# Performance work log

Hardware: AMD Instinct MI355X
Metric: run time of the kernel (lower is better)

The kernel has to match this reference:

```python
import jax, jax.numpy as jnp
import numpy as np

B, C, F = 4, 512, 2048
N, H = 8, 64  # header_size, header_channels
ALPHA = 1.0 / np.sqrt(H)


def setup_inputs() -> dict:
    key = jax.random.key(0)
    ks = jax.random.split(key, 6)
    return {
        "from_tensor": jax.random.normal(ks[0], (B, C, F), jnp.float32),
        "to_tensor": jax.random.normal(ks[1], (B, C, F), jnp.float32),
        "mask": jnp.ones((B, F, F), jnp.float32),
        "Wq": jax.random.normal(ks[2], (N * H, C), jnp.float32) * 0.02,
        "bq": jnp.zeros((N * H,), jnp.float32),
        "Wk": jax.random.normal(ks[3], (N * H, C), jnp.float32) * 0.02,
        "bk": jnp.zeros((N * H,), jnp.float32),
        "Wv": jax.random.normal(ks[4], (N * H, C), jnp.float32) * 0.02,
        "bv": jnp.zeros((N * H,), jnp.float32),
    }


def reference(from_tensor, to_tensor, mask, Wq, bq, Wk, bk, Wv, bv):
    b, _, f = from_tensor.shape
    t = to_tensor.shape[2]
    # Dense over channel dim: [B,C,F] -> [B,N*H,F], then split heads
    q = (jnp.einsum("oc,bcf->bof", Wq, from_tensor) + bq[None, :, None]).reshape(b, N, H, f)
    k = (jnp.einsum("oc,bct->bot", Wk, to_tensor) + bk[None, :, None]).reshape(b, N, H, t)
    v = (jnp.einsum("oc,bct->bot", Wv, to_tensor) + bv[None, :, None]).reshape(b, N, H, t)
    # score: q^T @ k -> [B,N,F,T]
    score = jnp.einsum("bnhf,bnht->bnft", q, k) * ALPHA
    score = score + (1.0 - mask[:, None]) * -100000.0
    probs = jax.nn.softmax(score, axis=-1)  # dropout=0 (inference)
    # context: probs @ v^T -> [B,N,F,H], transpose -> [B,N,H,F]
    ctx = jnp.einsum("bnft,bnht->bnhf", probs, v)
    return ctx.reshape(b, N * H, f)
```

## Files before the change

### kernel.cpp

```cpp
#include <hip/hip_runtime.h>

typedef __bf16 bf16x8 __attribute__((ext_vector_type(8)));
typedef float f32x4 __attribute__((ext_vector_type(4)));
typedef float f32x16 __attribute__((ext_vector_type(16)));
typedef unsigned short u16;
typedef u16 u16x8 __attribute__((ext_vector_type(8)));
typedef unsigned int u32;
typedef u32 u32x4 __attribute__((ext_vector_type(4)));
typedef unsigned long long u64;

#define DEVFN static __device__ __forceinline__

DEVFN u16 f2bf(float x) {
  u32 u = __builtin_bit_cast(u32, x);
  u32 r = u + 0x7FFFu + ((u >> 16) & 1u);
  return (u16)(r >> 16);
}

DEVFN float myexp2(float x) {
#if __has_builtin(__builtin_amdgcn_exp2f)
  return __builtin_amdgcn_exp2f(x);
#else
  return exp2f(x);
#endif
}

DEVFN u32 cvt_pk_bf16(float lo, float hi) {
  u32 r;
  asm("v_cvt_pk_bf16_f32 %0, %1, %2" : "=v"(r) : "v"(lo), "v"(hi));
  return r;
}

__global__ __launch_bounds__(256, 2) void proj_kernel(
    const float* __restrict__ from_t, const float* __restrict__ to_t,
    const float* __restrict__ Wq, const float* __restrict__ bq,
    const float* __restrict__ Wk, const float* __restrict__ bk,
    const float* __restrict__ Wv, const float* __restrict__ bv,
    u16* __restrict__ qt, u16* __restrict__ kt, u16* __restrict__ vt) {
  const int d     = blockIdx.x;
  const int xcd   = d & 7;
  const int b     = xcd >> 1;
  const int fh    = xcd & 1;
  const int local = d >> 3;
  const int mat   = local >> 5;
  const int o0    = ((local >> 3) & 3) * 128;
  const int f0    = (fh * 8 + (local & 7)) * 128;

  const float* X    = (mat == 0) ? from_t : to_t;
  const float* W    = (mat == 0) ? Wq : (mat == 1 ? Wk : Wv);
  const float* bias = (mat == 0) ? bq : (mat == 1 ? bk : bv);
  const bool isT = (mat < 2);

  __shared__ u16 Xs[128][64];
  __shared__ u16 Ws[128][64];

  const int tid  = threadIdx.x;
  const int lane = tid & 63;
  const int w    = tid >> 6;

  f32x4 acc[4][4];
#pragma unroll
  for (int i = 0; i < 4; ++i)
#pragma unroll
    for (int j = 0; j < 4; ++j)
#pragma unroll
      for (int r = 0; r < 4; ++r) acc[i][j][r] = 0.f;

  const int arow0 = (w & 1) * 64;
  const int brow0 = (w >> 1) * 64;

  for (int c0 = 0; c0 < 512; c0 += 64) {
    __syncthreads();
#pragma unroll
    for (int i = 0; i < 4; ++i) {
      const int task = tid + 256 * i;
      const int f = task & 127, cg = task >> 7;
      const float* xp = X + ((size_t)b * 512 + c0 + cg * 8) * 2048 + f0 + f;
      float xv[8];
#pragma unroll
      for (int j = 0; j < 8; ++j) xv[j] = xp[(size_t)j * 2048];
      u32x4 pk;
#pragma unroll
      for (int j = 0; j < 4; ++j) pk[j] = cvt_pk_bf16(xv[2 * j], xv[2 * j + 1]);
      *(u32x4*)&Xs[f][(cg ^ (f & 7)) * 8] = pk;
    }
#pragma unroll
    for (int i = 0; i < 4; ++i) {
      const int task = tid + 256 * i;
      const int o = task & 127, cg = task >> 7;
      const float* wp = W + (size_t)(o0 + o) * 512 + c0 + cg * 8;
      const float4 w0 = *(const float4*)(wp);
      const float4 w1 = *(const float4*)(wp + 4);
      u32x4 pk;
      pk[0] = cvt_pk_bf16(w0.x, w0.y);
      pk[1] = cvt_pk_bf16(w0.z, w0.w);
      pk[2] = cvt_pk_bf16(w1.x, w1.y);
      pk[3] = cvt_pk_bf16(w1.z, w1.w);
      *(u32x4*)&Ws[o][(cg ^ (o & 7)) * 8] = pk;
    }
    __syncthreads();

#pragma unroll
    for (int kk = 0; kk < 2; ++kk) {
      const int cb8 = kk * 4;
      bf16x8 afr[4], bfr[4];
#pragma unroll
      for (int mi = 0; mi < 4; ++mi) {
        const int row = arow0 + mi * 16 + (lane & 15);
        const int ch  = (cb8 + (lane >> 4)) ^ (row & 7);
        afr[mi] = *(const bf16x8*)&(isT ? Xs : Ws)[row][ch * 8];
      }
#pragma unroll
      for (int ni = 0; ni < 4; ++ni) {
        const int row = brow0 + ni * 16 + (lane & 15);
        const int ch  = (cb8 + (lane >> 4)) ^ (row & 7);
        bfr[ni] = *(const bf16x8*)&(isT ? Ws : Xs)[row][ch * 8];
      }
#pragma unroll
      for (int mi = 0; mi < 4; ++mi)
#pragma unroll
        for (int ni = 0; ni < 4; ++ni)
          acc[mi][ni] = __builtin_amdgcn_mfma_f32_16x16x32_bf16(
              afr[mi], bfr[ni], acc[mi][ni], 0, 0, 0);
    }
  }

  const float qscale = 0.18033688011112042f;
#pragma unroll
  for (int mi = 0; mi < 4; ++mi)
#pragma unroll
    for (int ni = 0; ni < 4; ++ni)
#pragma unroll
      for (int r = 0; r < 4; ++r) {
        const int rA = arow0 + mi * 16 + (lane >> 4) * 4 + r;
        const int cB = brow0 + ni * 16 + (lane & 15);
        int f, o;
        if (isT) { f = f0 + rA; o = o0 + cB; }
        else     { o = o0 + rA; f = f0 + cB; }
        float val = acc[mi][ni][r] + bias[o];
        if (mat == 0) val *= qscale;
        const u16 hv = f2bf(val);
        if (isT) {
          u16* dst = (mat == 0) ? qt : kt;
          dst[(((size_t)b * 8 + (o >> 6)) * 2048 + f) * 64 + (o & 63)] = hv;
        } else {
          vt[((size_t)b * 512 + o) * 2048 + f] = hv;
        }
      }
}

__global__ __launch_bounds__(256, 4) void maskflag_kernel(
    const float* __restrict__ mask, u32* __restrict__ fmask) {
  const int d    = blockIdx.x;
  const int b    = d >> 9;
  const int ft   = (d >> 5) & 15;
  const int tile = d & 31;
  const int t    = threadIdx.x;

  const float* base =
      mask + ((size_t)b * 2048 + ft * 128) * 2048 + tile * 64;
  bool ok = true;
#pragma unroll
  for (int i = 0; i < 8; ++i) {
    const int row = (t >> 4) * 8 + i;
    const float4 v = *(const float4*)(base + (size_t)row * 2048 + (t & 15) * 4);
    ok = ok && (v.x == 1.0f) && (v.y == 1.0f) && (v.z == 1.0f) && (v.w == 1.0f);
  }
  const u64 bal = __ballot(ok);
  __shared__ u32 wok[4];
  if ((t & 63) == 0) wok[t >> 6] = (bal == ~0ull) ? 1u : 0u;
  __syncthreads();
  if (t == 0) {
    const u32 allok = wok[0] & wok[1] & wok[2] & wok[3];
    if (allok) atomicOr(&fmask[b * 16 + ft], 1u << tile);
  }
}

#define SB __builtin_amdgcn_sched_barrier(0)

#define STAGE(BB, T0)                                                          \
  do {                                                                         \
    __builtin_amdgcn_global_load_lds(                                          \
        (const __attribute__((address_space(1))) void*)(ksrc1 + (size_t)(T0) * 64), \
        (__attribute__((address_space(3))) void*)&Ks[BB][w * 16][0], 16, 0, 0);\
    __builtin_amdgcn_global_load_lds(                                          \
        (const __attribute__((address_space(1))) void*)(ksrc2 + (size_t)(T0) * 64), \
        (__attribute__((address_space(3))) void*)&Ks[BB][w * 16 + 8][0], 16, 0, 0); \
    __builtin_amdgcn_global_load_lds(                                          \
        (const __attribute__((address_space(1))) void*)(vsrc1 + (T0)),         \
        (__attribute__((address_space(3))) void*)&Vs[BB][w * 16][0], 16, 0, 0);\
    __builtin_amdgcn_global_load_lds(                                          \
        (const __attribute__((address_space(1))) void*)(vsrc2 + (T0)),         \
        (__attribute__((address_space(3))) void*)&Vs[BB][w * 16 + 8][0], 16, 0, 0); \
  } while (0)

#define LDK(BUF)                                                               \
  do {                                                                         \
    _Pragma("unroll")                                                          \
    for (int kf_ = 0; kf_ < 4; ++kf_)                                          \
      _Pragma("unroll")                                                        \
      for (int mi_ = 0; mi_ < 2; ++mi_) {                                      \
        const int row_ = mi_ * 32 + fl;                                        \
        kreg[mi_][kf_] =                                                       \
            *(const bf16x8*)&Ks[BUF][row_][((kf_ * 2 + g) ^ (row_ & 7)) * 8];  \
      }                                                                        \
  } while (0)

#define LDV(BUF)                                                               \
  do {                                                                         \
    _Pragma("unroll")                                                          \
    for (int tf_ = 0; tf_ < 4; ++tf_)                                          \
      _Pragma("unroll")                                                        \
      for (int mh_ = 0; mh_ < 2; ++mh_) {                                      \
        const int row_ = mh_ * 32 + fl;                                        \
        vreg[mh_][tf_] =                                                       \
            *(const bf16x8*)&Vs[BUF][row_][((tf_ * 2 + g) ^ (row_ & 7)) * 8];  \
      }                                                                        \
  } while (0)

#define QKMM(SN)                                                               \
  do {                                                                         \
    _Pragma("unroll")                                                          \
    for (int m_ = 0; m_ < 2; ++m_)                                             \
      _Pragma("unroll")                                                        \
      for (int r_ = 0; r_ < 16; ++r_) SN[m_][r_] = 0.f;                        \
    _Pragma("unroll")                                                          \
    for (int kf_ = 0; kf_ < 4; ++kf_)                                          \
      _Pragma("unroll")                                                        \
      for (int mi_ = 0; mi_ < 2; ++mi_)                                        \
        SN[mi_] = __builtin_amdgcn_mfma_f32_32x32x16_bf16(kreg[mi_][kf_],      \
                                                          qf[kf_], SN[mi_],    \
                                                          0, 0, 0);            \
  } while (0)

#define ROUND(RB, SC, SN, T0)                                                  \
  {                                                                            \
    asm volatile("s_waitcnt vmcnt(0)" ::: "memory");                           \
    SB;                                                                        \
    __builtin_amdgcn_s_barrier();                                              \
    SB;                                                                        \
    LDV(RB);                                                                   \
    LDK((RB + 1) & 3);                                                         \
    SB;                                                                        \
    STAGE((RB + 2) & 3, ((T0) + 128) & 2047);                                  \
    SB;                                                                        \
    QKMM(SN);           \
                  \
    if (!((fmask >> ((T0) >> 6)) & 1u)) {                                      \
      float4 mk[8];                                                            \
      _Pragma("unroll")                                                        \
      for (int i_ = 0; i_ < 8; ++i_)                                           \
        mk[i_] = *(const float4*)(mrow + (T0) + (i_ >> 2) * 32 +               \
                                  (i_ & 3) * 8 + g * 4);                       \
      _Pragma("unroll")                                                        \
      for (int mi = 0; mi < 2; ++mi)                                           \
        _Pragma("unroll")                                                      \
        for (int q = 0; q < 4; ++q) {                                          \
          const float4 mv = mk[mi * 4 + q];                                    \
          SC[mi][q * 4 + 0] = fmaf(mv.x - 1.f, 144269.50408889634f, SC[mi][q * 4 + 0]); \
          SC[mi][q * 4 + 1] = fmaf(mv.y - 1.f, 144269.50408889634f, SC[mi][q * 4 + 1]); \
          SC[mi][q * 4 + 2] = fmaf(mv.z - 1.f, 144269.50408889634f, SC[mi][q * 4 + 2]); \
          SC[mi][q * 4 + 3] = fmaf(mv.w - 1.f, 144269.50408889634f, SC[mi][q * 4 + 3]); \
        }                                                                      \
    }                                                                          \
    float ps0 = 0.f, ps1 = 0.f, ps2 = 0.f, ps3 = 0.f;                          \
    _Pragma("unroll")                                                          \
    for (int mi = 0; mi < 2; ++mi)                                             \
      _Pragma("unroll")                                                        \
      for (int r = 0; r < 16; r += 4) {                                        \
        SC[mi][r + 0] = myexp2(SC[mi][r + 0]); ps0 += SC[mi][r + 0];           \
        SC[mi][r + 1] = myexp2(SC[mi][r + 1]); ps1 += SC[mi][r + 1];           \
        SC[mi][r + 2] = myexp2(SC[mi][r + 2]); ps2 += SC[mi][r + 2];           \
        SC[mi][r + 3] = myexp2(SC[mi][r + 3]); ps3 += SC[mi][r + 3];           \
      }                                                                        \
    {                                                                          \
      float ps = (ps0 + ps1) + (ps2 + ps3);                                    \
      ps += __shfl_xor(ps, 32, 64);                                            \
      L += ps;                                                                 \
    }                                                                          \
        \
    u32 dwv[2][4][2];                                                          \
    _Pragma("unroll")                                                          \
    for (int mi = 0; mi < 2; ++mi)                                             \
      _Pragma("unroll")                                                        \
      for (int q = 0; q < 4; ++q) {                                            \
        dwv[mi][q][0] = cvt_pk_bf16(SC[mi][q * 4 + 0], SC[mi][q * 4 + 1]);     \
        dwv[mi][q][1] = cvt_pk_bf16(SC[mi][q * 4 + 2], SC[mi][q * 4 + 3]);     \
      }                                                                        \
    _Pragma("unroll")                                                          \
    for (int tf = 0; tf < 4; ++tf) {                                           \
      const int m_ = tf >> 1, bq2 = tf & 1;                                    \
      u32 A0 = dwv[m_][bq2 * 2][0], A1 = dwv[m_][bq2 * 2][1];                  \
      u32 C0 = dwv[m_][bq2 * 2 + 1][0], C1 = dwv[m_][bq2 * 2 + 1][1];          \
      asm("v_permlane32_swap_b32 %0, %1" : "+v"(A0), "+v"(C0));                \
      asm("v_permlane32_swap_b32 %0, %1" : "+v"(A1), "+v"(C1));                \
      u32x4 pw; pw[0] = A0; pw[1] = A1; pw[2] = C0; pw[3] = C1;                \
      const bf16x8 pfr = __builtin_bit_cast(bf16x8, pw);                       \
      _Pragma("unroll")                                                        \
      for (int mih = 0; mih < 2; ++mih)                                        \
        ctx[mih] = __builtin_amdgcn_mfma_f32_32x32x16_bf16(vreg[mih][tf], pfr, \
                                                           ctx[mih], 0, 0, 0); \
    }                                                                          \
  }

__global__ __launch_bounds__(256, 2) void attn_kernel(
    const float* __restrict__ mask, const u32* __restrict__ fmaskbuf,
    const u16* __restrict__ qt, const u16* __restrict__ kt,
    const u16* __restrict__ vt, float* __restrict__ out) {
  const int d     = blockIdx.x;
  const int xcd   = d & 7;
  const int b     = xcd >> 1;
  const int fthi  = xcd & 1;
  const int local = d >> 3;
  const int n     = local & 7;
  const int ft    = fthi * 8 + (local >> 3);

  const int tid  = threadIdx.x;
  const int lane = tid & 63;
  const int w    = tid >> 6;
  const int g    = lane >> 5;
  const int fl   = lane & 31;
  const int f    = ft * 128 + w * 32 + fl;

  const u16* qtb = qt + ((size_t)b * 8 + n) * 2048 * 64;
  const u16* ktb = kt + ((size_t)b * 8 + n) * 2048 * 64;
  const u16* vb  = vt + ((size_t)b * 512 + n * 64) * 2048;
  const float* mrow = mask + ((size_t)b * 2048 + f) * 2048;
  const u32 fmask = fmaskbuf ? fmaskbuf[b * 16 + ft] : 0u;

  __shared__ u16 Ks[4][64][64];
  __shared__ u16 Vs[4][64][64];

  bf16x8 qf[4];
#pragma unroll
  for (int kf = 0; kf < 4; ++kf)
    qf[kf] = *(const bf16x8*)(qtb + (size_t)f * 64 + kf * 16 + g * 8);

  f32x16 ctx[2];
#pragma unroll
  for (int m = 0; m < 2; ++m)
#pragma unroll
    for (int r = 0; r < 16; ++r) ctx[m][r] = 0.f;
  float L = 0.f;

  const int sr1 = w * 16 + (lane >> 3), sr2 = sr1 + 8;
  const int sc1 = (lane & 7) ^ (sr1 & 7), sc2 = (lane & 7) ^ (sr2 & 7);
  const u16* ksrc1 = ktb + (size_t)sr1 * 64 + sc1 * 8;
  const u16* ksrc2 = ktb + (size_t)sr2 * 64 + sc2 * 8;
  const u16* vsrc1 = vb + (size_t)sr1 * 2048 + sc1 * 8;
  const u16* vsrc2 = vb + (size_t)sr2 * 2048 + sc2 * 8;

  bf16x8 kreg[2][4], vreg[2][4];
  f32x16 sA[2], sB[2];

  STAGE(0, 0);
  STAGE(1, 64);
  SB;
  asm volatile("s_waitcnt vmcnt(0)" ::: "memory");
  SB;
  __builtin_amdgcn_s_barrier();
  SB;
  LDK(0);
  QKMM(sA);

  for (int t0 = 0; t0 < 2048; t0 += 256) {
    ROUND(0, sA, sB, t0);
    ROUND(1, sB, sA, t0 + 64);
    ROUND(2, sA, sB, t0 + 128);
    ROUND(3, sB, sA, t0 + 192);
  }

  const float Linv = 1.0f / L;
#pragma unroll
  for (int mih = 0; mih < 2; ++mih)
#pragma unroll
    for (int r = 0; r < 16; ++r) {
      const int h = mih * 32 + (r & 3) + 8 * (r >> 2) + 4 * g;
      out[((size_t)b * 512 + n * 64 + h) * 2048 + f] = ctx[mih][r] * Linv;
    }
}

extern "C" void kernel_launch(void* const* d_in, const int* in_sizes, int n_in,
                              void* d_out, int out_size, void* d_ws, size_t ws_size,
                              hipStream_t stream) {
  const float* from_t = (const float*)d_in[0];
  const float* to_t   = (const float*)d_in[1];
  const float* mask   = (const float*)d_in[2];
  const float* Wq     = (const float*)d_in[3];
  const float* bq     = (const float*)d_in[4];
  const float* Wk     = (const float*)d_in[5];
  const float* bk     = (const float*)d_in[6];
  const float* Wv     = (const float*)d_in[7];
  const float* bv     = (const float*)d_in[8];
  float* out = (float*)d_out;

  u16* qt = (u16*)d_ws;
  u16* kt = qt + (size_t)4 * 8 * 2048 * 64;
  u16* vt = kt + (size_t)4 * 8 * 2048 * 64;
  const size_t base = (size_t)24 * 1024 * 1024;
  u32* fl = (ws_size >= base + 256) ? (u32*)((char*)d_ws + base) : nullptr;

  proj_kernel<<<dim3(768), 256, 0, stream>>>(from_t, to_t, Wq, bq, Wk, bk,
                                             Wv, bv, qt, kt, vt);
  if (fl) {
    hipMemsetAsync(fl, 0, 64 * sizeof(u32), stream);
    maskflag_kernel<<<dim3(2048), 256, 0, stream>>>(mask, fl);
  }
  attn_kernel<<<dim3(512), 256, 0, stream>>>(mask, fl, qt, kt, vt, out);
}
```

Measured before the change: 116.2 us.

## Fuse mask-flag scan into projection kernel and software-pipeline projection loads

Merges the mask-flag scanning kernel into the projection kernel. The grid is interleaved so each XCD runs 3 GEMM blocks for every 8 mask-scan blocks, which removes one kernel launch and lets the memory-bound mask reads overlap with projection compute. The projection loop is also double-buffered in registers: the next K-slice's global loads are issued before the current slice's MFMAs. This raises register pressure and adds an extra barrier per iteration.

```diff
diff --git a/kernel.cpp b/kernel.cpp
--- a/kernel.cpp
+++ b/kernel.cpp
@@ -31,17 +31,103 @@
   return r;
 }
 
-__global__ __launch_bounds__(256, 2) void proj_kernel(
+#define PLOADX(S)                                                              \
+  do {                                                                         \
+    _Pragma("unroll")                                                          \
+    for (int i = 0; i < 4; ++i) {                                              \
+      const int task = tid + 256 * i;                                          \
+      const int fq = task & 127, cg = task >> 7;                               \
+      const float* xp =                                                        \
+          X + ((size_t)b * 512 + (S)*64 + cg * 8) * 2048 + f0 + fq;            \
+      _Pragma("unroll")                                                        \
+      for (int j = 0; j < 8; ++j) xv[i][j] = xp[(size_t)j * 2048];             \
+    }                                                                          \
+  } while (0)
+
+#define PLOADW(S)                                                              \
+  do {                                                                         \
+    _Pragma("unroll")                                                          \
+    for (int i = 0; i < 4; ++i) {                                              \
+      const int task = tid + 256 * i;                                          \
+      const int o = task & 127, cg = task >> 7;                                \
+      const float* wp = W + (size_t)(o0 + o) * 512 + (S)*64 + cg * 8;          \
+      wv[i][0] = *(const float4*)wp;                                           \
+      wv[i][1] = *(const float4*)(wp + 4);                                     \
+    }                                                                          \
+  } while (0)
+
+#define PWRITE()                                                               \
+  do {                                                                         \
+    _Pragma("unroll")                                                          \
+    for (int i = 0; i < 4; ++i) {                                              \
+      const int task = tid + 256 * i;                                          \
+      const int fq = task & 127, cg = task >> 7;                               \
+      u32x4 pk;                                                                \
+      _Pragma("unroll")                                                        \
+      for (int j = 0; j < 4; ++j)                                              \
+        pk[j] = cvt_pk_bf16(xv[i][2 * j], xv[i][2 * j + 1]);                   \
+      *(u32x4*)&Xs[fq][(cg ^ (fq & 7)) * 8] = pk;                              \
+    }                                                                          \
+    _Pragma("unroll")                                                          \
+    for (int i = 0; i < 4; ++i) {                                              \
+      const int task = tid + 256 * i;                                          \
+      const int o = task & 127, cg = task >> 7;                                \
+      u32x4 pk;                                                                \
+      pk[0] = cvt_pk_bf16(wv[i][0].x, wv[i][0].y);                             \
+      pk[1] = cvt_pk_bf16(wv[i][0].z, wv[i][0].w);                             \
+      pk[2] = cvt_pk_bf16(wv[i][1].x, wv[i][1].y);                             \
+      pk[3] = cvt_pk_bf16(wv[i][1].z, wv[i][1].w);                             \
+      *(u32x4*)&Ws[o][(cg ^ (o & 7)) * 8] = pk;                                \
+    }                                                                          \
+  } while (0)
+
+__global__ __launch_bounds__(256, 2) void projflag_kernel(
     const float* __restrict__ from_t, const float* __restrict__ to_t,
+    const float* __restrict__ mask,
     const float* __restrict__ Wq, const float* __restrict__ bq,
     const float* __restrict__ Wk, const float* __restrict__ bk,
     const float* __restrict__ Wv, const float* __restrict__ bv,
-    u16* __restrict__ qt, u16* __restrict__ kt, u16* __restrict__ vt) {
-  const int d     = blockIdx.x;
-  const int xcd   = d & 7;
+    u16* __restrict__ qt, u16* __restrict__ kt, u16* __restrict__ vt,
+    u32* __restrict__ fmask) {
+  __shared__ u16 Xs[128][64];
+  __shared__ u16 Ws[128][64];
+
+  const int bid = blockIdx.x;
+  const int xcd = bid & 7;
+  const int li  = bid >> 3;
+  const int grp = li / 11, rem = li % 11;
+  const int tid = threadIdx.x;
+
+  if (rem >= 3) {
+    if (!fmask) return;
+    const int fi   = xcd * 256 + grp * 8 + (rem - 3);
+    const int b    = fi >> 9;
+    const int ft   = (fi >> 5) & 15;
+    const int tile = fi & 31;
+    const float* base =
+        mask + ((size_t)b * 2048 + ft * 128) * 2048 + tile * 64;
+    bool ok = true;
+#pragma unroll
+    for (int i = 0; i < 8; ++i) {
+      const int row = (tid >> 4) * 8 + i;
+      const float4 v =
+          *(const float4*)(base + (size_t)row * 2048 + (tid & 15) * 4);
+      ok = ok && (v.x == 1.0f) && (v.y == 1.0f) && (v.z == 1.0f) && (v.w == 1.0f);
+    }
+    const u64 bal = __ballot(ok);
+    u32* wok = (u32*)&Xs[0][0];
+    if ((tid & 63) == 0) wok[tid >> 6] = (bal == ~0ull) ? 1u : 0u;
+    __syncthreads();
+    if (tid == 0) {
+      const u32 allok = wok[0] & wok[1] & wok[2] & wok[3];
+      if (allok) atomicOr(&fmask[b * 16 + ft], 1u << tile);
+    }
+    return;
+  }
+
   const int b     = xcd >> 1;
   const int fh    = xcd & 1;
-  const int local = d >> 3;
+  const int local = grp * 3 + rem;
   const int mat   = local >> 5;
   const int o0    = ((local >> 3) & 3) * 128;
   const int f0    = (fh * 8 + (local & 7)) * 128;
@@ -51,10 +137,6 @@
   const float* bias = (mat == 0) ? bq : (mat == 1 ? bk : bv);
   const bool isT = (mat < 2);
 
-  __shared__ u16 Xs[128][64];
-  __shared__ u16 Ws[128][64];
-
-  const int tid  = threadIdx.x;
   const int lane = tid & 63;
   const int w    = tid >> 6;
 
@@ -69,37 +151,20 @@
   const int arow0 = (w & 1) * 64;
   const int brow0 = (w >> 1) * 64;
 
-  for (int c0 = 0; c0 < 512; c0 += 64) {
-    __syncthreads();
-#pragma unroll
-    for (int i = 0; i < 4; ++i) {
-      const int task = tid + 256 * i;
-      const int f = task & 127, cg = task >> 7;
-      const float* xp = X + ((size_t)b * 512 + c0 + cg * 8) * 2048 + f0 + f;
-      float xv[8];
-#pragma unroll
-      for (int j = 0; j < 8; ++j) xv[j] = xp[(size_t)j * 2048];
-      u32x4 pk;
-#pragma unroll
-      for (int j = 0; j < 4; ++j) pk[j] = cvt_pk_bf16(xv[2 * j], xv[2 * j + 1]);
-      *(u32x4*)&Xs[f][(cg ^ (f & 7)) * 8] = pk;
+  float  xv[4][8];
+  float4 wv[4][2];
+
+  PLOADX(0);
+  PLOADW(0);
+  PWRITE();
+  __syncthreads();
+
+#pragma unroll
+  for (int s = 0; s < 8; ++s) {
+    if (s < 7) {
+      PLOADX(s + 1);
+      PLOADW(s + 1);
     }
-#pragma unroll
-    for (int i = 0; i < 4; ++i) {
-      const int task = tid + 256 * i;
-      const int o = task & 127, cg = task >> 7;
-      const float* wp = W + (size_t)(o0 + o) * 512 + c0 + cg * 8;
-      const float4 w0 = *(const float4*)(wp);
-      const float4 w1 = *(const float4*)(wp + 4);
-      u32x4 pk;
-      pk[0] = cvt_pk_bf16(w0.x, w0.y);
-      pk[1] = cvt_pk_bf16(w0.z, w0.w);
-      pk[2] = cvt_pk_bf16(w1.x, w1.y);
-      pk[3] = cvt_pk_bf16(w1.z, w1.w);
-      *(u32x4*)&Ws[o][(cg ^ (o & 7)) * 8] = pk;
-    }
-    __syncthreads();
-
 #pragma unroll
     for (int kk = 0; kk < 2; ++kk) {
       const int cb8 = kk * 4;
@@ -123,6 +188,9 @@
           acc[mi][ni] = __builtin_amdgcn_mfma_f32_16x16x32_bf16(
               afr[mi], bfr[ni], acc[mi][ni], 0, 0, 0);
     }
+    __syncthreads();
+    if (s < 7) PWRITE();
+    __syncthreads();
   }
 
   const float qscale = 0.18033688011112042f;
@@ -149,33 +217,6 @@
       }
 }
 
-__global__ __launch_bounds__(256, 4) void maskflag_kernel(
-    const float* __restrict__ mask, u32* __restrict__ fmask) {
-  const int d    = blockIdx.x;
-  const int b    = d >> 9;
-  const int ft   = (d >> 5) & 15;
-  const int tile = d & 31;
-  const int t    = threadIdx.x;
-
-  const float* base =
-      mask + ((size_t)b * 2048 + ft * 128) * 2048 + tile * 64;
-  bool ok = true;
-#pragma unroll
-  for (int i = 0; i < 8; ++i) {
-    const int row = (t >> 4) * 8 + i;
-    const float4 v = *(const float4*)(base + (size_t)row * 2048 + (t & 15) * 4);
-    ok = ok && (v.x == 1.0f) && (v.y == 1.0f) && (v.z == 1.0f) && (v.w == 1.0f);
-  }
-  const u64 bal = __ballot(ok);
-  __shared__ u32 wok[4];
-  if ((t & 63) == 0) wok[t >> 6] = (bal == ~0ull) ? 1u : 0u;
-  __syncthreads();
-  if (t == 0) {
-    const u32 allok = wok[0] & wok[1] & wok[2] & wok[3];
-    if (allok) atomicOr(&fmask[b * 16 + ft], 1u << tile);
-  }
-}
-
 #define SB __builtin_amdgcn_sched_barrier(0)
 
 #define STAGE(BB, T0)                                                          \
@@ -400,11 +441,8 @@
   const size_t base = (size_t)24 * 1024 * 1024;
   u32* fl = (ws_size >= base + 256) ? (u32*)((char*)d_ws + base) : nullptr;
 
-  proj_kernel<<<dim3(768), 256, 0, stream>>>(from_t, to_t, Wq, bq, Wk, bk,
-                                             Wv, bv, qt, kt, vt);
-  if (fl) {
-    hipMemsetAsync(fl, 0, 64 * sizeof(u32), stream);
-    maskflag_kernel<<<dim3(2048), 256, 0, stream>>>(mask, fl);
-  }
+  if (fl) hipMemsetAsync(fl, 0, 64 * sizeof(u32), stream);
+  projflag_kernel<<<dim3(2816), 256, 0, stream>>>(
+      from_t, to_t, mask, Wq, bq, Wk, bk, Wv, bv, qt, kt, vt, fl);
   attn_kernel<<<dim3(512), 256, 0, stream>>>(mask, fl, qt, kt, vt, out);
 }
```

Measured after the change: 134.5 us. +15.7%, slower.
